# Performance work log

Hardware: AMD Instinct MI355X
Metric: run time of the kernel (lower is better)

Reference implementation:

```python
import jax, jax.numpy as jnp
import numpy as np

B, S, D, H = 4, 2048, 1024, 16
DK = D // H


def setup_inputs() -> dict:
    key = jax.random.key(0)
    ks = jax.random.split(key, 7)
    scale = 0.02
    return {
        "q": jax.random.normal(ks[0], (B, S, D), jnp.float32),
        "k": jax.random.normal(ks[1], (B, S, D), jnp.float32),
        "v": jax.random.normal(ks[2], (B, S, D), jnp.float32),
        "mask": jnp.ones((B, 1, S, S), dtype=bool),
        "w_q": jax.random.normal(ks[3], (D, D), jnp.float32) * scale,
        "w_k": jax.random.normal(ks[4], (D, D), jnp.float32) * scale,
        "w_v": jax.random.normal(ks[5], (D, D), jnp.float32) * scale,
        "w_o": jax.random.normal(ks[6], (D, D), jnp.float32) * scale,
    }


def reference(q, k, v, mask, w_q, w_k, w_v, w_o):
    # Linear projections (torch nn.Linear: y = x @ W^T, bias=False)
    def split_heads(x, w):
        y = jnp.einsum('bsd,ed->bse', x, w)            # [B,S,D]
        return y.reshape(x.shape[0], x.shape[1], H, DK).transpose(0, 2, 1, 3)  # [B,H,S,DK]

    qh = split_heads(q, w_q)
    kh = split_heads(k, w_k)
    vh = split_heads(v, w_v)

    scores = jnp.einsum('bhqd,bhkd->bhqk', qh, kh) / jnp.sqrt(jnp.float32(DK))  # [B,H,S,S]
    scores = jnp.where(mask, scores, jnp.float32(-1e9))
    attn = jax.nn.softmax(scores, axis=-1)
    # dropout p=0.0 -> identity (eval mode)
    out = jnp.einsum('bhqk,bhkd->bhqd', attn, vh)      # [B,H,S,DK]
    out = out.transpose(0, 2, 1, 3).reshape(out.shape[0], out.shape[2], D)     # [B,S,D]
    return jnp.einsum('bsd,ed->bse', out, w_o)         # output projection
```

## Files before the change

### kernel.cpp

```cpp
#include <hip/hip_runtime.h>
#include <hip/hip_bf16.h>
#include <stdint.h>

typedef __bf16 bf16;
typedef __bf16 bf16x8 __attribute__((ext_vector_type(8)));
typedef float f32x4 __attribute__((ext_vector_type(4)));
typedef float f32x16 __attribute__((ext_vector_type(16)));
typedef unsigned short u16;
typedef u16 u16x8 __attribute__((ext_vector_type(8)));
typedef unsigned int u32;
typedef u32 u32x2 __attribute__((ext_vector_type(2)));
typedef u32 u32x4 __attribute__((ext_vector_type(4)));

#define GLOAD16(g, l)                                                          \
  __builtin_amdgcn_global_load_lds(                                            \
      (const __attribute__((address_space(1))) void*)(g),                      \
      (__attribute__((address_space(3))) void*)(l), 16, 0, 0)

static constexpr int BB = 4, SS = 2048, DD = 1024, HH = 16, DKH = 64;
static constexpr int NTOK = BB * SS;
static constexpr float KSC = 0.125f * 1.44269504f;

__device__ __forceinline__ u32 cvtpk_bf16(float a, float b) {
  u32 r;
  asm("v_cvt_pk_bf16_f32 %0, %1, %2" : "=v"(r) : "v"(a), "v"(b));
  return r;
}
#define PLSWAP(a, b) asm("v_permlane32_swap_b32 %0, %1" : "+v"(a), "+v"(b))

__global__ __launch_bounds__(256) void cast_w(const float* __restrict__ w0,
                                              const float* __restrict__ w1,
                                              const float* __restrict__ w2,
                                              const float* __restrict__ w3,
                                              bf16* __restrict__ dst) {
  const int bid = (int)blockIdx.x;
  const int wsel = bid >> 9;
  const int blk = bid & 511;
  const float* src = wsel == 0 ? w0 : wsel == 1 ? w1 : wsel == 2 ? w2 : w3;
  const size_t base = (size_t)blk * 2048 + (size_t)threadIdx.x * 8;
  f32x4 a = *(const f32x4*)(src + base);
  f32x4 b = *(const f32x4*)(src + base + 4);
  bf16x8 o;
#pragma unroll
  for (int j = 0; j < 4; ++j) { o[j] = (bf16)a[j]; o[j + 4] = (bf16)b[j]; }
  *(bf16x8*)(dst + (size_t)wsel * 1048576 + base) = o;
}

__global__ __launch_bounds__(256, 2) void gemm_proj(const float* __restrict__ Aq,
                                                    const float* __restrict__ Ak,
                                                    const float* __restrict__ Avv,
                                                    const bf16* __restrict__ Wb,
                                                    bf16* __restrict__ Cq,
                                                    bf16* __restrict__ Ck,
                                                    bf16* __restrict__ Cv) {
  __shared__ __align__(16) char smem[32 * 1024];
  char* As = smem;
  char* Bs = smem + 16 * 1024;
  const int tid = threadIdx.x;
  const int lane = tid & 63;
  const int wid = tid >> 6;
  const int wr = wid >> 1, wc = wid & 1;

  const int bid0 = (int)blockIdx.x;
  const int g = bid0 >> 9;
  int bid = bid0 & 511;
  bid = (bid & 7) * 64 + (bid >> 3);
  const float* A = g == 0 ? Aq : g == 1 ? Ak : Avv;
  const bf16* W = Wb + (size_t)g * 1048576;
  bf16* C = g == 0 ? Cq : g == 1 ? Ck : Cv;
  const float cs = g == 0 ? KSC : 1.0f;
  const int bm = (bid >> 3) << 7;
  const int bn = (bid & 7) << 7;

  const int r_ld = tid >> 3;
  const int cb_ld = (tid & 7) << 4;
  const int lrow = lane & 15;
  const int lk16 = (lane >> 4) << 4;

  f32x4 acc[4][4] = {};

  for (int kt = 0; kt < 1024; kt += 64) {
#pragma unroll
    for (int i = 0; i < 4; ++i) {
      const int row = i * 32 + r_ld;
      const float* src = A + (size_t)(bm + row) * 1024 + kt + ((tid & 7) * 8);
      f32x4 a = *(const f32x4*)src;
      f32x4 b = *(const f32x4*)(src + 4);
      bf16x8 o;
#pragma unroll
      for (int j = 0; j < 4; ++j) { o[j] = (bf16)a[j]; o[j + 4] = (bf16)b[j]; }
      *(bf16x8*)(As + row * 128 + (cb_ld ^ ((row & 7) << 4))) = o;
    }
#pragma unroll
    for (int i = 0; i < 4; ++i) {
      const int row = i * 32 + r_ld;
      const int scb = cb_ld ^ ((row & 7) << 4);
      GLOAD16((const char*)(W + (size_t)(bn + row) * 1024 + kt) + scb,
              Bs + i * 4096 + wid * 1024);
    }
    asm volatile("s_waitcnt vmcnt(0)" ::: "memory");
    __syncthreads();
#pragma unroll
    for (int ks = 0; ks < 2; ++ks) {
      bf16x8 af[4], bfr[4];
#pragma unroll
      for (int m = 0; m < 4; ++m) {
        const int row = wr * 64 + m * 16 + lrow;
        const int cb = (ks * 64 + lk16) ^ ((row & 7) << 4);
        af[m] = *(const bf16x8*)(As + row * 128 + cb);
      }
#pragma unroll
      for (int n = 0; n < 4; ++n) {
        const int row = wc * 64 + n * 16 + lrow;
        const int cb = (ks * 64 + lk16) ^ ((row & 7) << 4);
        bfr[n] = *(const bf16x8*)(Bs + row * 128 + cb);
      }
#pragma unroll
      for (int m = 0; m < 4; ++m)
#pragma unroll
        for (int n = 0; n < 4; ++n)
          acc[m][n] = __builtin_amdgcn_mfma_f32_16x16x32_bf16(af[m], bfr[n],
                                                              acc[m][n], 0, 0, 0);
    }
    __syncthreads();
  }

#pragma unroll
  for (int m = 0; m < 4; ++m) {
    const int row0 = bm + wr * 64 + m * 16 + ((lane >> 4) << 2);
#pragma unroll
    for (int n = 0; n < 4; ++n) {
      const int col = bn + wc * 64 + n * 16 + lrow;
#pragma unroll
      for (int r = 0; r < 4; ++r)
        C[(size_t)(row0 + r) * 1024 + col] = (bf16)(acc[m][n][r] * cs);
    }
  }
}

__global__ __launch_bounds__(256, 2) void gemm_out(const bf16* __restrict__ A,
                                                   const bf16* __restrict__ W,
                                                   float* __restrict__ C) {
  __shared__ __align__(16) char smem[32 * 1024];
  char* As = smem;
  char* Bs = smem + 16 * 1024;
  const int tid = threadIdx.x;
  const int lane = tid & 63;
  const int wid = tid >> 6;
  const int wr = wid >> 1, wc = wid & 1;
  int bid = (int)blockIdx.x;
  bid = (bid & 7) * 64 + (bid >> 3);
  const int bm = (bid >> 3) << 7;
  const int bn = (bid & 7) << 7;

  const int r_ld = tid >> 3;
  const int cb_ld = (tid & 7) << 4;
  const int lrow = lane & 15;
  const int lk16 = (lane >> 4) << 4;

  f32x4 acc[4][4] = {};

  for (int kt = 0; kt < 1024; kt += 64) {
#pragma unroll
    for (int i = 0; i < 4; ++i) {
      const int row = i * 32 + r_ld;
      const int scb = cb_ld ^ ((row & 7) << 4);
      GLOAD16((const char*)(A + (size_t)(bm + row) * 1024 + kt) + scb,
              As + i * 4096 + wid * 1024);
      GLOAD16((const char*)(W + (size_t)(bn + row) * 1024 + kt) + scb,
              Bs + i * 4096 + wid * 1024);
    }
    asm volatile("s_waitcnt vmcnt(0)" ::: "memory");
    __syncthreads();
#pragma unroll
    for (int ks = 0; ks < 2; ++ks) {
      bf16x8 af[4], bfr[4];
#pragma unroll
      for (int m = 0; m < 4; ++m) {
        const int row = wr * 64 + m * 16 + lrow;
        const int cb = (ks * 64 + lk16) ^ ((row & 7) << 4);
        af[m] = *(const bf16x8*)(As + row * 128 + cb);
      }
#pragma unroll
      for (int n = 0; n < 4; ++n) {
        const int row = wc * 64 + n * 16 + lrow;
        const int cb = (ks * 64 + lk16) ^ ((row & 7) << 4);
        bfr[n] = *(const bf16x8*)(Bs + row * 128 + cb);
      }
#pragma unroll
      for (int m = 0; m < 4; ++m)
#pragma unroll
        for (int n = 0; n < 4; ++n)
          acc[m][n] = __builtin_amdgcn_mfma_f32_16x16x32_bf16(af[m], bfr[n],
                                                              acc[m][n], 0, 0, 0);
    }
    __syncthreads();
  }

#pragma unroll
  for (int m = 0; m < 4; ++m) {
    const int row0 = bm + wr * 64 + m * 16 + ((lane >> 4) << 2);
#pragma unroll
    for (int n = 0; n < 4; ++n) {
      const int col = bn + wc * 64 + n * 16 + lrow;
#pragma unroll
      for (int r = 0; r < 4; ++r)
        C[(size_t)(row0 + r) * 1024 + col] = acc[m][n][r];
    }
  }
}

__global__ __launch_bounds__(256) void transpose_v(const bf16* __restrict__ vp,
                                                   bf16* __restrict__ vt) {
  __shared__ u16 T[64][68];
  const int bid = (int)blockIdx.x;
  const int bh = bid >> 5;
  const int st = bid & 31;
  const int b = bh >> 4, h = bh & 15;
  const int tid = threadIdx.x;
  const int s0 = st << 6;
  const u16* src = (const u16*)vp + (size_t)(b * SS + s0) * DD + h * DKH;
#pragma unroll
  for (int i = 0; i < 2; ++i) {
    const int row = i * 32 + (tid >> 3);
    const int c0 = (tid & 7) * 8;
    u16x8 v = *(const u16x8*)(src + (size_t)row * DD + c0);
#pragma unroll
    for (int j = 0; j < 8; ++j) T[row][c0 + j] = v[j];
  }
  __syncthreads();
  u16* dst = (u16*)vt + (size_t)bh * DKH * SS + s0;
#pragma unroll
  for (int i = 0; i < 2; ++i) {
    const int dk = i * 32 + (tid >> 3);
    const int sc = (tid & 7) * 8;
    u16x8 v;
#pragma unroll
    for (int j = 0; j < 8; ++j) v[j] = T[sc + j][dk];
    *(u16x8*)(dst + (size_t)dk * SS + sc) = v;
  }
}

__global__ __launch_bounds__(256, 4) void attn_fwd(const bf16* __restrict__ qp,
                                                   const bf16* __restrict__ kp,
                                                   const bf16* __restrict__ vt,
                                                   bf16* __restrict__ ao) {
  __shared__ __align__(16) char smem[32 * 1024];

  const int tid = threadIdx.x;
  const int lane = tid & 63;
  const int wid = tid >> 6;
  const int l31 = lane & 31;
  const int hi = lane >> 5;
  const int hi16 = hi << 4;

  const int bid = (int)blockIdx.x;
  const int xcd = bid & 7, idx = bid >> 3;
  const int bh = xcd * 8 + (idx >> 4);
  const int qt = idx & 15;
  const int b = bh >> 4, h = bh & 15;
  const int q0 = qt << 7;

  const bf16* qrow = qp + (size_t)(b * SS + q0 + wid * 32 + l31) * DD + h * DKH;
  bf16x8 qf[4];
#pragma unroll
  for (int st = 0; st < 4; ++st)
    qf[st] = *(const bf16x8*)(qrow + st * 16 + hi * 8);

  f32x16 o[2] = {};
  f32x16 lacc = {};
  bf16x8 ones;
#pragma unroll
  for (int j = 0; j < 8; ++j) ones[j] = (bf16)1.0f;

  const char* ksrc = (const char*)(kp + (size_t)b * SS * DD + h * DKH);
  const char* vsrc = (const char*)(vt + (size_t)bh * DKH * SS);
  const int srow = tid >> 3;
  const int scol16 = (tid & 7) << 4;

#define STAGE(KV0, BUFB)                                                       \
  {                                                                            \
    _Pragma("unroll") for (int i = 0; i < 2; ++i) {                            \
      const int row = i * 32 + srow;                                           \
      const int sc = scol16 ^ ((row & 7) << 4);                                \
      GLOAD16(ksrc + (size_t)((KV0) + row) * 2048 + sc,                        \
              smem + (BUFB) + i * 4096 + wid * 1024);                          \
      GLOAD16(vsrc + (size_t)row * 4096 + (size_t)(KV0) * 2 + sc,              \
              smem + (BUFB) + 8192 + i * 4096 + wid * 1024);                   \
    }                                                                          \
  }

  STAGE(0, 0);
  asm volatile("s_waitcnt vmcnt(0)" ::: "memory");
  __syncthreads();

  const int NT = SS / 64;
  for (int t = 0; t < NT; ++t) {
    const int cur = (t & 1) * 16384;
    if (t + 1 < NT) STAGE((t + 1) * 64, cur ^ 16384);

    const char* Kb = smem + cur;
    const char* Vb = Kb + 8192;

    f32x16 s[2] = {};
    __builtin_amdgcn_s_setprio(1);
#pragma unroll
    for (int st = 0; st < 4; ++st)
#pragma unroll
      for (int sub = 0; sub < 2; ++sub) {
        const int row = sub * 32 + l31;
        bf16x8 kf = *(const bf16x8*)(Kb + row * 128 +
                                     ((st * 32 + hi16) ^ ((row & 7) << 4)));
        s[sub] = __builtin_amdgcn_mfma_f32_32x32x16_bf16(kf, qf[st], s[sub],
                                                         0, 0, 0);
      }
    __builtin_amdgcn_s_setprio(0);

#pragma unroll
    for (int sub = 0; sub < 2; ++sub)
#pragma unroll
      for (int r = 0; r < 16; ++r) s[sub][r] = exp2f(s[sub][r]);

    bf16x8 pa[4];
#pragma unroll
    for (int ks = 0; ks < 4; ++ks) {
      const int sub = ks >> 1, bse = (ks & 1) * 8;
      u32 a0 = cvtpk_bf16(s[sub][bse + 0], s[sub][bse + 1]);
      u32 b0 = cvtpk_bf16(s[sub][bse + 4], s[sub][bse + 5]);
      PLSWAP(a0, b0);
      u32 a1 = cvtpk_bf16(s[sub][bse + 2], s[sub][bse + 3]);
      u32 b1 = cvtpk_bf16(s[sub][bse + 6], s[sub][bse + 7]);
      PLSWAP(a1, b1);
      union { u32x4 w; bf16x8 v; } u;
      u.w[0] = a0; u.w[1] = a1; u.w[2] = b0; u.w[3] = b1;
      pa[ks] = u.v;
    }

    __builtin_amdgcn_s_setprio(1);
#pragma unroll
    for (int da = 0; da < 2; ++da)
#pragma unroll
      for (int ks = 0; ks < 4; ++ks) {
        const int row = da * 32 + l31;
        bf16x8 vf = *(const bf16x8*)(Vb + row * 128 +
                                     ((ks * 32 + hi16) ^ ((row & 7) << 4)));
        o[da] = __builtin_amdgcn_mfma_f32_32x32x16_bf16(vf, pa[ks], o[da],
                                                        0, 0, 0);
      }
#pragma unroll
    for (int ks = 0; ks < 4; ++ks)
      lacc = __builtin_amdgcn_mfma_f32_32x32x16_bf16(ones, pa[ks], lacc,
                                                     0, 0, 0);
    __builtin_amdgcn_s_setprio(0);

    asm volatile("s_waitcnt vmcnt(0)" ::: "memory");
    __syncthreads();
  }

  char* ow = smem + wid * 4096;
  {
    const float inv = 1.0f / lacc[0];
    const int q = l31;
    const int swz = (q & 7) << 4;
#pragma unroll
    for (int da = 0; da < 2; ++da)
#pragma unroll
      for (int g = 0; g < 4; ++g) {
        u32x2 pr;
        pr[0] = cvtpk_bf16(o[da][g * 4 + 0] * inv, o[da][g * 4 + 1] * inv);
        pr[1] = cvtpk_bf16(o[da][g * 4 + 2] * inv, o[da][g * 4 + 3] * inv);
        *(u32x2*)(ow + q * 128 + ((da * 64 + g * 16 + hi * 8) ^ swz)) = pr;
      }
  }
  __syncthreads();
#pragma unroll
  for (int p = 0; p < 4; ++p) {
    const int qb = p * 32 + (tid >> 3);
    const int w = qb >> 5, ql = qb & 31;
    bf16x8 v = *(const bf16x8*)(smem + w * 4096 + ql * 128 +
                                (((tid & 7) << 4) ^ ((ql & 7) << 4)));
    *(bf16x8*)(ao + (size_t)(b * SS + q0 + qb) * DD + h * DKH + (tid & 7) * 8) = v;
  }
#undef STAGE
}

extern "C" void kernel_launch(void* const* d_in, const int* in_sizes, int n_in,
                              void* d_out, int out_size, void* d_ws,
                              size_t ws_size, hipStream_t stream) {
  const float* q  = (const float*)d_in[0];
  const float* k  = (const float*)d_in[1];
  const float* v  = (const float*)d_in[2];
  const float* wq = (const float*)d_in[4];
  const float* wk = (const float*)d_in[5];
  const float* wv = (const float*)d_in[6];
  const float* wo = (const float*)d_in[7];
  float* out = (float*)d_out;

  const size_t T = (size_t)NTOK * DD;
  bf16* wb = (bf16*)d_ws;
  bf16* qp = wb + 4 * 1048576;
  bf16* kp = qp + T;
  bf16* vp = kp + T;
  bf16* vtb = vp + T;
  bf16* ao = vp;

  dim3 blk(256);
  cast_w<<<dim3(2048), blk, 0, stream>>>(wq, wk, wv, wo, wb);
  gemm_proj<<<dim3(1536), blk, 0, stream>>>(q, k, v, wb, qp, kp, vp);
  transpose_v<<<dim3(2048), blk, 0, stream>>>(vp, vtb);
  attn_fwd<<<dim3(1024), blk, 0, stream>>>(qp, kp, vtb, ao);
  gemm_out<<<dim3(512), blk, 0, stream>>>(ao, wb + 3145728, out);
}
```

Baseline: 204.5 us.

## Emit transposed V from projection GEMM and compute softmax row sums in registers

The V projection now computes W_v·V^T by swapping the operand roles, so it writes V already transposed ([D, B*S]) and the separate transpose_v kernel and its launch are removed. In attention, the softmax denominator is now built from a register reduction plus a cross-lane shuffle instead of extra MFMAs against a ones vector. This cuts one full pass over V in global memory and four MFMAs per tile, at the cost of VALU reduction work and a different store pattern in the V GEMM epilogue.

```diff
diff --git a/kernel.cpp b/kernel.cpp
--- a/kernel.cpp
+++ b/kernel.cpp
@@ -48,11 +48,11 @@
 
 __global__ __launch_bounds__(256, 2) void gemm_proj(const float* __restrict__ Aq,
                                                     const float* __restrict__ Ak,
-                                                    const float* __restrict__ Avv,
+                                                    const float* __restrict__ Av_,
                                                     const bf16* __restrict__ Wb,
                                                     bf16* __restrict__ Cq,
                                                     bf16* __restrict__ Ck,
-                                                    bf16* __restrict__ Cv) {
+                                                    bf16* __restrict__ Cvt) {
   __shared__ __align__(16) char smem[32 * 1024];
   char* As = smem;
   char* Bs = smem + 16 * 1024;
@@ -65,12 +65,22 @@
   const int g = bid0 >> 9;
   int bid = bid0 & 511;
   bid = (bid & 7) * 64 + (bid >> 3);
-  const float* A = g == 0 ? Aq : g == 1 ? Ak : Avv;
-  const bf16* W = Wb + (size_t)g * 1048576;
-  bf16* C = g == 0 ? Cq : g == 1 ? Ck : Cv;
-  const float cs = g == 0 ? KSC : 1.0f;
-  const int bm = (bid >> 3) << 7;
-  const int bn = (bid & 7) << 7;
+
+  const float* Af32;
+  const bf16* Bbf;
+  bf16* Cp;
+  float cs = 1.0f;
+  if (g == 0)      { Af32 = Aq;  Bbf = Wb;           Cp = Cq;  cs = KSC; }
+  else if (g == 1) { Af32 = Ak;  Bbf = Wb + 1048576; Cp = Ck; }
+  else             { Af32 = Av_; Bbf = Wb + 2097152; Cp = Cvt; }
+
+  const int bm = (g == 2) ? (bid & 7) << 7 : (bid >> 3) << 7;
+  const int bn = (g == 2) ? (bid >> 3) << 7 : (bid & 7) << 7;
+  const int f32base = (g == 2) ? bn : bm;
+  const int bfbase  = (g == 2) ? bm : bn;
+  char* f32dst = (g == 2) ? Bs : As;
+  char* bfdst  = (g == 2) ? As : Bs;
+  const size_t cN = (g == 2) ? 8192 : 1024;
 
   const int r_ld = tid >> 3;
   const int cb_ld = (tid & 7) << 4;
@@ -83,20 +93,20 @@
 #pragma unroll
     for (int i = 0; i < 4; ++i) {
       const int row = i * 32 + r_ld;
-      const float* src = A + (size_t)(bm + row) * 1024 + kt + ((tid & 7) * 8);
+      const float* src = Af32 + (size_t)(f32base + row) * 1024 + kt + ((tid & 7) * 8);
       f32x4 a = *(const f32x4*)src;
       f32x4 b = *(const f32x4*)(src + 4);
       bf16x8 o;
 #pragma unroll
       for (int j = 0; j < 4; ++j) { o[j] = (bf16)a[j]; o[j + 4] = (bf16)b[j]; }
-      *(bf16x8*)(As + row * 128 + (cb_ld ^ ((row & 7) << 4))) = o;
+      *(bf16x8*)(f32dst + row * 128 + (cb_ld ^ ((row & 7) << 4))) = o;
     }
 #pragma unroll
     for (int i = 0; i < 4; ++i) {
       const int row = i * 32 + r_ld;
       const int scb = cb_ld ^ ((row & 7) << 4);
-      GLOAD16((const char*)(W + (size_t)(bn + row) * 1024 + kt) + scb,
-              Bs + i * 4096 + wid * 1024);
+      GLOAD16((const char*)(Bbf + (size_t)(bfbase + row) * 1024 + kt) + scb,
+              bfdst + i * 4096 + wid * 1024);
     }
     asm volatile("s_waitcnt vmcnt(0)" ::: "memory");
     __syncthreads();
@@ -133,7 +143,7 @@
       const int col = bn + wc * 64 + n * 16 + lrow;
 #pragma unroll
       for (int r = 0; r < 4; ++r)
-        C[(size_t)(row0 + r) * 1024 + col] = (bf16)(acc[m][n][r] * cs);
+        Cp[(size_t)(row0 + r) * cN + col] = (bf16)(acc[m][n][r] * cs);
     }
   }
 }
@@ -210,40 +220,9 @@
   }
 }
 
-__global__ __launch_bounds__(256) void transpose_v(const bf16* __restrict__ vp,
-                                                   bf16* __restrict__ vt) {
-  __shared__ u16 T[64][68];
-  const int bid = (int)blockIdx.x;
-  const int bh = bid >> 5;
-  const int st = bid & 31;
-  const int b = bh >> 4, h = bh & 15;
-  const int tid = threadIdx.x;
-  const int s0 = st << 6;
-  const u16* src = (const u16*)vp + (size_t)(b * SS + s0) * DD + h * DKH;
-#pragma unroll
-  for (int i = 0; i < 2; ++i) {
-    const int row = i * 32 + (tid >> 3);
-    const int c0 = (tid & 7) * 8;
-    u16x8 v = *(const u16x8*)(src + (size_t)row * DD + c0);
-#pragma unroll
-    for (int j = 0; j < 8; ++j) T[row][c0 + j] = v[j];
-  }
-  __syncthreads();
-  u16* dst = (u16*)vt + (size_t)bh * DKH * SS + s0;
-#pragma unroll
-  for (int i = 0; i < 2; ++i) {
-    const int dk = i * 32 + (tid >> 3);
-    const int sc = (tid & 7) * 8;
-    u16x8 v;
-#pragma unroll
-    for (int j = 0; j < 8; ++j) v[j] = T[sc + j][dk];
-    *(u16x8*)(dst + (size_t)dk * SS + sc) = v;
-  }
-}
-
 __global__ __launch_bounds__(256, 4) void attn_fwd(const bf16* __restrict__ qp,
                                                    const bf16* __restrict__ kp,
-                                                   const bf16* __restrict__ vt,
+                                                   const bf16* __restrict__ vt2,
                                                    bf16* __restrict__ ao) {
   __shared__ __align__(16) char smem[32 * 1024];
 
@@ -268,13 +247,10 @@
     qf[st] = *(const bf16x8*)(qrow + st * 16 + hi * 8);
 
   f32x16 o[2] = {};
-  f32x16 lacc = {};
-  bf16x8 ones;
-#pragma unroll
-  for (int j = 0; j < 8; ++j) ones[j] = (bf16)1.0f;
+  float l = 0.f;
 
   const char* ksrc = (const char*)(kp + (size_t)b * SS * DD + h * DKH);
-  const char* vsrc = (const char*)(vt + (size_t)bh * DKH * SS);
+  const char* vsrc = (const char*)vt2 + (size_t)h * 64 * 16384 + (size_t)b * 4096;
   const int srow = tid >> 3;
   const int scol16 = (tid & 7) << 4;
 
@@ -285,7 +261,7 @@
       const int sc = scol16 ^ ((row & 7) << 4);                                \
       GLOAD16(ksrc + (size_t)((KV0) + row) * 2048 + sc,                        \
               smem + (BUFB) + i * 4096 + wid * 1024);                          \
-      GLOAD16(vsrc + (size_t)row * 4096 + (size_t)(KV0) * 2 + sc,              \
+      GLOAD16(vsrc + (size_t)row * 16384 + (size_t)(KV0) * 2 + sc,             \
               smem + (BUFB) + 8192 + i * 4096 + wid * 1024);                   \
     }                                                                          \
   }
@@ -320,6 +296,18 @@
     for (int sub = 0; sub < 2; ++sub)
 #pragma unroll
       for (int r = 0; r < 16; ++r) s[sub][r] = exp2f(s[sub][r]);
+
+    float red[16];
+#pragma unroll
+    for (int r = 0; r < 16; ++r) red[r] = s[0][r] + s[1][r];
+#pragma unroll
+    for (int stp = 8; stp >= 1; stp >>= 1)
+#pragma unroll
+      for (int i = 0; i < 8; ++i)
+        if (i < stp) red[i] += red[i + stp];
+    float rs = red[0];
+    rs += __shfl_xor(rs, 32);
+    l += rs;
 
     bf16x8 pa[4];
 #pragma unroll
@@ -347,10 +335,6 @@
         o[da] = __builtin_amdgcn_mfma_f32_32x32x16_bf16(vf, pa[ks], o[da],
                                                         0, 0, 0);
       }
-#pragma unroll
-    for (int ks = 0; ks < 4; ++ks)
-      lacc = __builtin_amdgcn_mfma_f32_32x32x16_bf16(ones, pa[ks], lacc,
-                                                     0, 0, 0);
     __builtin_amdgcn_s_setprio(0);
 
     asm volatile("s_waitcnt vmcnt(0)" ::: "memory");
@@ -359,7 +343,7 @@
 
   char* ow = smem + wid * 4096;
   {
-    const float inv = 1.0f / lacc[0];
+    const float inv = 1.0f / l;
     const int q = l31;
     const int swz = (q & 7) << 4;
 #pragma unroll
@@ -397,17 +381,15 @@
   float* out = (float*)d_out;
 
   const size_t T = (size_t)NTOK * DD;
-  bf16* wb = (bf16*)d_ws;
-  bf16* qp = wb + 4 * 1048576;
-  bf16* kp = qp + T;
-  bf16* vp = kp + T;
-  bf16* vtb = vp + T;
-  bf16* ao = vp;
+  bf16* wb  = (bf16*)d_ws;
+  bf16* qp  = wb + 4 * 1048576;
+  bf16* kp  = qp + T;
+  bf16* vt2 = kp + T;
+  bf16* ao  = vt2 + T;
 
   dim3 blk(256);
   cast_w<<<dim3(2048), blk, 0, stream>>>(wq, wk, wv, wo, wb);
-  gemm_proj<<<dim3(1536), blk, 0, stream>>>(q, k, v, wb, qp, kp, vp);
-  transpose_v<<<dim3(2048), blk, 0, stream>>>(vp, vtb);
-  attn_fwd<<<dim3(1024), blk, 0, stream>>>(qp, kp, vtb, ao);
+  gemm_proj<<<dim3(1536), blk, 0, stream>>>(q, k, v, wb, qp, kp, vt2);
+  attn_fwd<<<dim3(1024), blk, 0, stream>>>(qp, kp, vt2, ao);
   gemm_out<<<dim3(512), blk, 0, stream>>>(ao, wb + 3145728, out);
 }
```

After: 189.5 us. -7.4%, faster.
